# Optimization experiments

Hardware: AMD Instinct MI355X
Metric: run time of the kernel (lower is better)

The kernel has to match this reference:

```python
import jax, jax.numpy as jnp
import numpy as np

HEADS = 8
MEM_LEN = 32


def _mha(q, k, v, Wq, bq, Wk, bk, Wv, bv, Wo, bo):
    # torch nn.MultiheadAttention, batch_first=False. q: [Lq,B,E], k/v: [Lk,B,E]
    Lq, B, E = q.shape
    d = E // HEADS

    def proj(t, W, b):
        p = t @ W.T + b
        return p.reshape(t.shape[0], B, HEADS, d).transpose(1, 2, 0, 3)  # [B,h,L,d]

    qh, kh, vh = proj(q, Wq, bq), proj(k, Wk, bk), proj(v, Wv, bv)
    scale = 1.0 / jnp.sqrt(jnp.asarray(d, q.dtype))
    att = jax.nn.softmax(jnp.einsum('bhqd,bhkd->bhqk', qh * scale, kh), axis=-1)
    out = jnp.einsum('bhqk,bhkd->bhqd', att, vh)          # [B,h,Lq,d]
    out = out.transpose(2, 0, 1, 3).reshape(Lq, B, E)
    return out @ Wo.T + bo


def _forward(x, h, c, memK, memV, externalK, externalV,
             W_ih, W_hh, b_ih, b_hh,
             sWq, sbq, sWk, sbk, sWv, sbv, sWo, sbo,
             cWq, cbq, cWk, cbk, cWv, cbv, cWo, cbo,
             Wres, bres, Wrout, brout, Wcomp, bcomp, Wexp, bexp, Wgate, bgate):
    H = h.shape[1]
    # LSTMCell (torch gate order i, f, g, o)
    gates = x @ W_ih.T + b_ih + h @ W_hh.T + b_hh
    i, f, g, o = jnp.split(gates, 4, axis=1)
    c_next = jax.nn.sigmoid(f) * c + jax.nn.sigmoid(i) * jnp.tanh(g)
    h_lstm = jax.nn.sigmoid(o) * jnp.tanh(c_next)
    # append detached h_lstm to short memory, keep last MEM_LEN entries
    cur = jax.lax.stop_gradient(h_lstm)[None]                      # [1,B,H]
    memK_new = jnp.concatenate([memK, cur], axis=0)[-MEM_LEN:]     # [ML,B,H]
    memV_new = jnp.concatenate([memV, cur], axis=0)[-MEM_LEN:]
    qSelf = h_lstm[None]                                           # [1,B,H]
    self_out = _mha(qSelf, memK_new, memV_new, sWq, sbq, sWk, sbk, sWv, sbv, sWo, sbo)[0]
    ext_out = _mha(qSelf, externalK, externalV, cWq, cbq, cWk, cbk, cWv, cbv, cWo, cbo)[0]
    rw = jax.nn.softmax(h_lstm @ Wrout.T + brout, axis=1)          # [B,2] router
    routed_attn = rw[:, :1] * self_out + rw[:, 1:2] * ext_out
    routed = h_lstm + routed_attn + routed_attn @ Wres.T + bres
    temporal_summary = memK_new.mean(axis=0)                       # [B,H]
    compressed = temporal_summary @ Wcomp.T + bcomp                # [B,H//4]
    expanded = compressed @ Wexp.T + bexp                          # [B,H]
    reps = -(-H // compressed.shape[1])
    compressed_expanded = jnp.tile(compressed, (1, reps))[:, :H]
    gate = jax.nn.sigmoid(jnp.concatenate([x, routed], axis=1) @ Wgate.T + bgate)
    hCT = compressed_expanded + gate * (expanded - compressed_expanded)  # torch.lerp
    hFinal = (h_lstm + routed + hCT) / 3.0                         # dropout = identity (eval)
    return hFinal, h_lstm, c_next


def setup_inputs() -> dict:
    key = jax.random.key(0)
    ks = jax.random.split(key, 34)
    B, I, H, ML, EL = 2048, 1024, 1024, 32, 32
    BN = H // 4
    rn = lambda k, s, sc=1.0: jax.random.normal(k, s, dtype=jnp.float32) * sc
    return {
        'x': rn(ks[0], (B, I)), 'h': rn(ks[1], (B, H)), 'c': rn(ks[2], (B, H)),
        'memK': rn(ks[3], (ML, B, H)), 'memV': rn(ks[4], (ML, B, H)),
        'externalK': rn(ks[5], (EL, B, H)), 'externalV': rn(ks[6], (EL, B, H)),
        'W_ih': rn(ks[7], (4 * H, I), 0.02), 'W_hh': rn(ks[8], (4 * H, H), 0.02),
        'b_ih': jnp.zeros((4 * H,), jnp.float32), 'b_hh': jnp.zeros((4 * H,), jnp.float32),
        'sWq': rn(ks[9], (H, H), 0.02), 'sbq': rn(ks[10], (H,), 0.02),
        'sWk': rn(ks[11], (H, H), 0.02), 'sbk': rn(ks[12], (H,), 0.02),
        'sWv': rn(ks[13], (H, H), 0.02), 'sbv': rn(ks[14], (H,), 0.02),
        'sWo': rn(ks[15], (H, H), 0.02), 'sbo': rn(ks[16], (H,), 0.02),
        'cWq': rn(ks[17], (H, H), 0.02), 'cbq': rn(ks[18], (H,), 0.02),
        'cWk': rn(ks[19], (H, H), 0.02), 'cbk': rn(ks[20], (H,), 0.02),
        'cWv': rn(ks[21], (H, H), 0.02), 'cbv': rn(ks[22], (H,), 0.02),
        'cWo': rn(ks[23], (H, H), 0.02), 'cbo': rn(ks[24], (H,), 0.02),
        'Wres': rn(ks[25], (H, H), 0.02), 'bres': rn(ks[26], (H,), 0.02),
        'Wrout': rn(ks[27], (2, H), 0.02), 'brout': rn(ks[28], (2,), 0.02),
        'Wcomp': rn(ks[29], (BN, H), 0.02), 'bcomp': rn(ks[30], (BN,), 0.02),
        'Wexp': rn(ks[31], (H, BN), 0.02), 'bexp': rn(ks[32], (H,), 0.02),
        'Wgate': rn(ks[33], (H, I + H), 0.02), 'bgate': jnp.zeros((H,), jnp.float32),
    }


def reference(x, h, c, memK, memV, externalK, externalV,
              W_ih, W_hh, b_ih, b_hh,
              sWq, sbq, sWk, sbk, sWv, sbv, sWo, sbo,
              cWq, cbq, cWk, cbk, cWv, cbv, cWo, cbo,
              Wres, bres, Wrout, brout, Wcomp, bcomp, Wexp, bexp, Wgate, bgate):
    return _forward(x, h, c, memK, memV, externalK, externalV,
                    W_ih, W_hh, b_ih, b_hh,
                    sWq, sbq, sWk, sbk, sWv, sbv, sWo, sbo,
                    cWq, cbq, cWk, cbk, cWv, cbv, cWo, cbo,
                    Wres, bres, Wrout, brout, Wcomp, bcomp, Wexp, bexp, Wgate, bgate)
```

## Files before the change

kernel.cpp:

```cpp
#include <hip/hip_runtime.h>
#include <math.h>

typedef __attribute__((ext_vector_type(4))) float f32x4;
typedef __attribute__((ext_vector_type(8))) short bf16x8;
typedef __attribute__((ext_vector_type(4))) unsigned short u16x4;

__device__ __forceinline__ unsigned short f2bf(float f) {
  unsigned u = __builtin_bit_cast(unsigned, f);
  u += 0x7fffu + ((u >> 16) & 1u);
  return (unsigned short)(u >> 16);
}
__device__ __forceinline__ float bf2f(unsigned short s) {
  return __builtin_bit_cast(float, (unsigned)s << 16);
}
__device__ __forceinline__ float sigmoidf_(float x) { return 1.f / (1.f + __expf(-x)); }

template <int TN, int ACAT, int BCAT, int EPI, int ABF16, int OBF16>
__global__ __launch_bounds__(256) void gemm_k(
    const void* __restrict__ A1, const void* __restrict__ A1b, int lda1, long aZ,
    const void* __restrict__ A2, int lda2, int Ksplit,
    const float* __restrict__ B1, const float* __restrict__ B1b, int ldb1, long bZ,
    const float* __restrict__ B2, int ldb2,
    const float* __restrict__ bias1, const float* __restrict__ bias1b, long biasZ,
    const float* __restrict__ bias2,
    void* __restrict__ C, void* __restrict__ Cb, int ldc, long cZ,
    int K, int zs, float scale,
    const float* __restrict__ P0, const float* __restrict__ P1,
    const float* __restrict__ P2, const float* __restrict__ P3) {
  constexpr int NBI = TN / 32;
  __shared__ unsigned short As[2][128][32];
  __shared__ unsigned short Bs[2][TN][32];
  const int t = threadIdx.x;
  const int lane = t & 63;
  const int wave = t >> 6;
  const int wr = wave >> 1, wc = wave & 1;

  const unsigned gx = gridDim.x, gy = gridDim.y;
  unsigned L = blockIdx.x + gx * (blockIdx.y + gy * blockIdx.z);
  const unsigned nwg = gx * gy * gridDim.z;
  L = (L & 7u) * (nwg >> 3) + (L >> 3);
  const int bn = L % gx;
  const unsigned r1 = L / gx;
  const int bm = r1 % gy;
  const int z = r1 / gy;

  const bool hi = z >= zs;
  const int zz = hi ? z - zs : z;
  const char* Abase = (const char*)(hi ? A1b : A1) + (long)zz * aZ * (ABF16 ? 2 : 4);
  const float* Bbase = (hi ? B1b : B1) + (long)zz * bZ;
  const float* biasp = hi ? bias1b : bias1;
  char* Czc = (char*)(hi ? Cb : C) + (long)zz * cZ * (OBF16 ? 2 : 4);

  const int ar = t >> 3;
  const int bc = (t & 7) * 4;

  const int kIters = K >> 5;
  u16x4 Ra[4], Rb[NBI];

  auto loadT = [&](int kt) {
    const int k0 = kt << 5;
    const char* Ap; int ldA, kA;
    if (ACAT == 1 && k0 >= Ksplit) { Ap = (const char*)A2; ldA = lda2; kA = k0 - Ksplit; }
    else { Ap = Abase; ldA = lda1; kA = k0; }
    const float* Bp; int ldB, kB;
    if (BCAT == 1 && k0 >= Ksplit) { Bp = B2; ldB = ldb2; kB = k0 - Ksplit; }
    else { Bp = Bbase; ldB = ldb1; kB = k0; }
#pragma unroll
    for (int i = 0; i < 4; ++i) {
      const long aoff = ((long)bm * 128 + ar + 32 * i) * ldA + kA + bc;
      if (ABF16) {
        Ra[i] = *(const u16x4*)((const unsigned short*)Ap + aoff);
      } else {
        f32x4 v = *(const f32x4*)((const float*)Ap + aoff);
        u16x4 pk;
        pk[0] = f2bf(v[0]); pk[1] = f2bf(v[1]); pk[2] = f2bf(v[2]); pk[3] = f2bf(v[3]);
        Ra[i] = pk;
      }
    }
#pragma unroll
    for (int i = 0; i < NBI; ++i) {
      f32x4 bv = *(const f32x4*)(Bp + ((long)bn * TN + ar + 32 * i) * ldB + kB + bc);
      u16x4 bp;
      bp[0] = f2bf(bv[0]); bp[1] = f2bf(bv[1]); bp[2] = f2bf(bv[2]); bp[3] = f2bf(bv[3]);
      Rb[i] = bp;
    }
  };

  loadT(0);

  f32x4 acc[4][NBI] = {};
  int p = 0;
  for (int kt = 0; kt < kIters; ++kt) {
    __syncthreads();
#pragma unroll
    for (int i = 0; i < 4; ++i) *(u16x4*)&As[p][ar + 32 * i][bc] = Ra[i];
#pragma unroll
    for (int i = 0; i < NBI; ++i) *(u16x4*)&Bs[p][ar + 32 * i][bc] = Rb[i];
    if (kt + 1 < kIters) loadT(kt + 1);
    __syncthreads();

    bf16x8 af[4], bfr[NBI];
#pragma unroll
    for (int mi = 0; mi < 4; ++mi)
      af[mi] = *(const bf16x8*)&As[p][wr * 64 + mi * 16 + (lane & 15)][(lane >> 4) * 8];
#pragma unroll
    for (int ni = 0; ni < NBI; ++ni)
      bfr[ni] = *(const bf16x8*)&Bs[p][wc * (TN / 2) + ni * 16 + (lane & 15)][(lane >> 4) * 8];
#pragma unroll
    for (int mi = 0; mi < 4; ++mi)
#pragma unroll
      for (int ni = 0; ni < NBI; ++ni)
        acc[mi][ni] = __builtin_amdgcn_mfma_f32_16x16x32_bf16(af[mi], bfr[ni], acc[mi][ni], 0, 0, 0);
    p ^= 1;
  }

  const int colb = bn * TN + wc * (TN / 2);
  const int rowb = bm * 128 + wr * 64;
#pragma unroll
  for (int mi = 0; mi < 4; ++mi) {
#pragma unroll
    for (int ni = 0; ni < NBI; ++ni) {
      f32x4 v = acc[mi][ni];
      const int col = colb + ni * 16 + (lane & 15);
      const int row0 = rowb + mi * 16 + ((lane >> 4) << 2);
      float bsum = 0.f;
      if (biasp) bsum += biasp[zz * biasZ + col];
      if (bias2) bsum += bias2[col];
#pragma unroll
      for (int q = 0; q < 4; ++q) {
        const long row = row0 + q;
        const long off = row * ldc + col;
        const float val = v[q] + bsum;
        if (EPI == 0) {
          if (OBF16) ((unsigned short*)Czc)[off] = f2bf(val * scale);
          else       ((float*)Czc)[off] = val * scale;
        } else if (EPI == 1) {
          ((float*)Czc)[off] = val + P0[off] + P1[off];
        } else if (EPI == 2) {
          const float g = sigmoidf_(val);
          const float ce = P0[row * 256 + (col & 255)];
          const float ex = P1[off];
          ((float*)Czc)[off] = (P2[off] + P3[off] + ce + g * (ex - ce)) * (1.f / 3.f);
        } else if (EPI == 3) {
          ((unsigned short*)Czc)[off] = f2bf(val * P0[2 * row + (hi ? 1 : 0)]);
        } else {
          ((float*)Czc)[off] = val + P2[2 * row] * P0[col] + P2[2 * row + 1] * P1[col];
        }
      }
    }
  }
}

__global__ __launch_bounds__(256) void transpose_k(const float* __restrict__ in0,
                                                   float* __restrict__ out0,
                                                   const float* __restrict__ in1,
                                                   float* __restrict__ out1, int n) {
  __shared__ float tile[64][65];
  const float* in = blockIdx.z ? in1 : in0;
  float* out = blockIdx.z ? out1 : out0;
  const int tr = blockIdx.y, tc = blockIdx.x, t = threadIdx.x;
#pragma unroll
  for (int it = 0; it < 16; ++it) {
    int idx = t + 256 * it;
    int r = idx >> 6, c = idx & 63;
    tile[r][c] = in[(long)(tr * 64 + r) * n + tc * 64 + c];
  }
  __syncthreads();
#pragma unroll
  for (int it = 0; it < 16; ++it) {
    int idx = t + 256 * it;
    int rr = idx >> 6, cc = idx & 63;
    out[(long)(tc * 64 + rr) * n + tr * 64 + cc] = tile[cc][rr];
  }
}

__global__ __launch_bounds__(256) void lstm_k(const float* __restrict__ gates,
                                              const float* __restrict__ c_in,
                                              const float* __restrict__ Wr,
                                              const float* __restrict__ br,
                                              float* __restrict__ c_out,
                                              float* __restrict__ h_ws,
                                              float* __restrict__ h_out,
                                              float* __restrict__ rw) {
  const int b = blockIdx.x, t = threadIdx.x;
  const long base = (long)b * 1024 + t * 4;
  const float* gb = gates + (long)b * 4096 + t * 4;
  f32x4 gi = *(const f32x4*)(gb);
  f32x4 gf = *(const f32x4*)(gb + 1024);
  f32x4 gg = *(const f32x4*)(gb + 2048);
  f32x4 go = *(const f32x4*)(gb + 3072);
  f32x4 cv = *(const f32x4*)(c_in + base);
  f32x4 cn, hv;
#pragma unroll
  for (int q = 0; q < 4; ++q) {
    float cc = sigmoidf_(gf[q]) * cv[q] + sigmoidf_(gi[q]) * tanhf(gg[q]);
    cn[q] = cc;
    hv[q] = sigmoidf_(go[q]) * tanhf(cc);
  }
  *(f32x4*)(c_out + base) = cn;
  *(f32x4*)(h_ws + base) = hv;
  *(f32x4*)(h_out + base) = hv;
  f32x4 w0 = *(const f32x4*)(Wr + t * 4);
  f32x4 w1 = *(const f32x4*)(Wr + 1024 + t * 4);
  float a0 = hv[0] * w0[0] + hv[1] * w0[1] + hv[2] * w0[2] + hv[3] * w0[3];
  float a1 = hv[0] * w1[0] + hv[1] * w1[1] + hv[2] * w1[2] + hv[3] * w1[3];
#pragma unroll
  for (int m = 32; m >= 1; m >>= 1) {
    a0 += __shfl_xor(a0, m);
    a1 += __shfl_xor(a1, m);
  }
  __shared__ float red[8];
  if ((t & 63) == 0) { red[t >> 6] = a0; red[4 + (t >> 6)] = a1; }
  __syncthreads();
  if (t == 0) {
    float z0 = red[0] + red[1] + red[2] + red[3] + br[0];
    float z1 = red[4] + red[5] + red[6] + red[7] + br[1];
    float mx = fmaxf(z0, z1);
    float e0 = __expf(z0 - mx), e1 = __expf(z1 - mx);
    float s = e0 + e1;
    rw[2 * b] = e0 / s;
    rw[2 * b + 1] = e1 / s;
  }
}

__global__ __launch_bounds__(256) void attn4_k(
    const float* __restrict__ memK, const float* __restrict__ memV,
    const float* __restrict__ extK, const float* __restrict__ extV,
    const float* __restrict__ hl,
    const unsigned short* __restrict__ qtS, const unsigned short* __restrict__ qtE,
    unsigned short* __restrict__ mixS, unsigned short* __restrict__ mixE,
    float* __restrict__ ts) {
  const int NB = 2048, H = 1024;
  __shared__ __align__(16) unsigned short LDSU[38912];
  __shared__ __align__(16) unsigned short P_lds[16 * 36];
  const int b = blockIdx.x;
  const bool self = blockIdx.y == 0;
  const int t = threadIdx.x, lane = t & 63, w = t >> 6;

  auto krow = [&](int r) -> const float* {
    return self ? ((r < 31) ? memK + ((long)(r + 1) * NB + b) * H : hl + (long)b * H)
                : extK + ((long)r * NB + b) * H;
  };
  auto vrow = [&](int r) -> const float* {
    return self ? ((r < 31) ? memV + ((long)(r + 1) * NB + b) * H : hl + (long)b * H)
                : extV + ((long)r * NB + b) * H;
  };

  const int chS = t >> 5, c4S = t & 31;
  const unsigned kbase = (unsigned)(chS * 4 + (c4S >> 3)) * 1168 + (unsigned)(c4S & 7) * 4;
#pragma unroll
  for (int g = 0; g < 4; ++g) {
    f32x4 R[8];
#pragma unroll
    for (int u = 0; u < 8; ++u) R[u] = *(const f32x4*)(krow(g * 8 + u) + t * 4);
#pragma unroll
    for (int u = 0; u < 8; ++u) {
      const int r = g * 8 + u;
      u16x4 pk;
      pk[0] = f2bf(R[u][0]); pk[1] = f2bf(R[u][1]); pk[2] = f2bf(R[u][2]); pk[3] = f2bf(R[u][3]);
      *(u16x4*)&LDSU[kbase + (unsigned)r * 36] = pk;
    }
  }
  __syncthreads();

  if (self) {
#pragma unroll
    for (int ci = 0; ci < 4; ++ci) {
      const int g = t + 256 * ci;
      const int q = g & 127;
      const unsigned short* base = &LDSU[(unsigned)((g >> 7) * 4 + (q >> 5)) * 1168 + (q & 31)];
      float s = 0.f;
#pragma unroll
      for (int r = 0; r < 32; ++r) s += bf2f(base[r * 36]);
      ts[(long)b * H + g] = s * (1.f / 32.f);
    }
  }

  const unsigned short* qtb =
      (self ? qtS : qtE) + (long)b * 8192 + (long)(lane & 7) * 1024 + (lane >> 4) * 8;
  f32x4 accS[2] = {};
  for (int jj = 0; jj < 32; ++jj) {
    bf16x8 bq = *(const bf16x8*)(qtb + jj * 32);
#pragma unroll
    for (int mi = 0; mi < 2; ++mi) {
      const unsigned short* ap =
          &LDSU[(unsigned)jj * 1168 + (unsigned)(mi * 16 + (lane & 15)) * 36 + (lane >> 4) * 8];
      union { unsigned long long q[2]; bf16x8 v; } ua;
      ua.q[0] = *(const unsigned long long*)ap;
      ua.q[1] = *(const unsigned long long*)(ap + 4);
      accS[mi] = __builtin_amdgcn_mfma_f32_16x16x32_bf16(ua.v, bq, accS[mi], 0, 0, 0);
    }
  }

  {
    float mx = -3.4e38f;
#pragma unroll
    for (int mi = 0; mi < 2; ++mi)
#pragma unroll
      for (int q = 0; q < 4; ++q) mx = fmaxf(mx, accS[mi][q]);
    mx = fmaxf(mx, __shfl_xor(mx, 16));
    mx = fmaxf(mx, __shfl_xor(mx, 32));
    float sum = 0.f;
    float pv[2][4];
#pragma unroll
    for (int mi = 0; mi < 2; ++mi)
#pragma unroll
      for (int q = 0; q < 4; ++q) { pv[mi][q] = __expf(accS[mi][q] - mx); sum += pv[mi][q]; }
    sum += __shfl_xor(sum, 16);
    sum += __shfl_xor(sum, 32);
    const float rinv = 1.f / sum;
    const bool valid = (lane & 15) < 8;
#pragma unroll
    for (int mi = 0; mi < 2; ++mi) {
      u16x4 pk;
#pragma unroll
      for (int q = 0; q < 4; ++q) pk[q] = valid ? f2bf(pv[mi][q] * rinv) : (unsigned short)0;
      *(u16x4*)&P_lds[(unsigned)(lane & 15) * 36 + mi * 16 + (lane >> 4) * 4] = pk;
    }
  }
  __syncthreads();

#pragma unroll
  for (int g = 0; g < 4; ++g) {
    f32x4 RA[4], RB[4];
#pragma unroll
    for (int u = 0; u < 4; ++u) {
      const int pr = g * 4 + u;
      RA[u] = *(const f32x4*)(vrow(2 * pr) + t * 4);
      RB[u] = *(const f32x4*)(vrow(2 * pr + 1) + t * 4);
    }
#pragma unroll
    for (int u = 0; u < 4; ++u) {
      const int pr = g * 4 + u;
#pragma unroll
      for (int e = 0; e < 4; ++e) {
        const unsigned dw = (unsigned)f2bf(RA[u][e]) | ((unsigned)f2bf(RB[u][e]) << 16);
        *(unsigned*)&LDSU[(unsigned)(t * 4 + e) * 38 + 2 * pr] = dw;
      }
    }
  }
  __syncthreads();

  bf16x8 pa = *(const bf16x8*)&P_lds[(unsigned)(lane & 15) * 36 + (lane >> 4) * 8];
  unsigned short* mixp = (self ? mixS : mixE) + (long)b * 8192;
#pragma unroll
  for (int ch = 0; ch < 8; ++ch) {
#pragma unroll
    for (int i = 0; i < 2; ++i) {
      const int dbase = ch * 128 + w * 32 + i * 16;
      const unsigned* vb =
          (const unsigned*)&LDSU[(unsigned)(dbase + (lane & 15)) * 38 + (lane >> 4) * 8];
      union { unsigned u[4]; bf16x8 v; } uu;
      uu.u[0] = vb[0]; uu.u[1] = vb[1]; uu.u[2] = vb[2]; uu.u[3] = vb[3];
      f32x4 o = __builtin_amdgcn_mfma_f32_16x16x32_bf16(pa, uu.v, (f32x4){0.f, 0.f, 0.f, 0.f},
                                                        0, 0, 0);
      if (lane < 32) {
        const int d = dbase + (lane & 15);
        const int h0 = (lane >> 4) * 4;
#pragma unroll
        for (int q = 0; q < 4; ++q) mixp[(long)(h0 + q) * 1024 + d] = f2bf(o[q]);
      }
    }
  }
}

extern "C" void kernel_launch(void* const* d_in, const int* in_sizes, int n_in,
                              void* d_out, int out_size, void* d_ws, size_t ws_size,
                              hipStream_t stream) {
  const float* x    = (const float*)d_in[0];
  const float* h    = (const float*)d_in[1];
  const float* c    = (const float*)d_in[2];
  const float* memK = (const float*)d_in[3];
  const float* memV = (const float*)d_in[4];
  const float* extK = (const float*)d_in[5];
  const float* extV = (const float*)d_in[6];
  const float* W_ih = (const float*)d_in[7];
  const float* W_hh = (const float*)d_in[8];
  const float* b_ih = (const float*)d_in[9];
  const float* b_hh = (const float*)d_in[10];
  const float* sWq = (const float*)d_in[11];
  const float* sbq = (const float*)d_in[12];
  const float* sWk = (const float*)d_in[13];
  const float* sWv = (const float*)d_in[15];
  const float* sbv = (const float*)d_in[16];
  const float* sWo = (const float*)d_in[17];
  const float* sbo = (const float*)d_in[18];
  const float* cWq = (const float*)d_in[19];
  const float* cbq = (const float*)d_in[20];
  const float* cWk = (const float*)d_in[21];
  const float* cWv = (const float*)d_in[23];
  const float* cbv = (const float*)d_in[24];
  const float* cWo = (const float*)d_in[25];
  const float* cbo = (const float*)d_in[26];
  const float* Wres = (const float*)d_in[27];
  const float* bres = (const float*)d_in[28];
  const float* Wrout = (const float*)d_in[29];
  const float* brout = (const float*)d_in[30];
  const float* Wcomp = (const float*)d_in[31];
  const float* bcomp = (const float*)d_in[32];
  const float* Wexp = (const float*)d_in[33];
  const float* bexp = (const float*)d_in[34];
  const float* Wgate = (const float*)d_in[35];
  const float* bgate = (const float*)d_in[36];
  (void)in_sizes; (void)n_in; (void)out_size; (void)ws_size;

  float* out = (float*)d_out;
  float* w = (float*)d_ws;
  const long M1 = 1024 * 1024;
  float* gates   = w;
  float* hl      = w + 8 * M1;
  unsigned short* qsS = (unsigned short*)(w + 10 * M1);
  unsigned short* qsE = (unsigned short*)(w + 12 * M1);
  float* wkTs    = w + 14 * M1;
  float* wkTc    = w + 15 * M1;
  unsigned short* qtS = (unsigned short*)(w + 16 * M1);
  unsigned short* qtE = (unsigned short*)(w + 32 * M1);
  unsigned short* mixS = (unsigned short*)(w + 48 * M1);
  unsigned short* mixE = (unsigned short*)(w + 64 * M1);
  float* ts      = w + 80 * M1;
  unsigned short* attnS = (unsigned short*)(w + 82 * M1);
  unsigned short* attnE = (unsigned short*)(w + 84 * M1);
  float* rw      = w + 90 * M1;
  float* rattn   = w + 91 * M1;
  float* routed  = w + 93 * M1;
  float* comp    = w + 95 * M1;
  float* expd    = w + 96 * M1;

  float* hFinal_out = out;
  float* hl_out     = out + 2 * M1;
  float* cn_out     = out + 4 * M1;

  const float scaleq = 0.08838834764831845f;
  const int ZBIG = 1 << 30;
  dim3 blk(256);
  const float* nf = nullptr;

  gemm_k<128, 1, 1, 0, 0, 0><<<dim3(32, 16, 1), blk, 0, stream>>>(
      x, nullptr, 1024, 0, h, 1024, 1024,
      W_ih, nf, 1024, 0, W_hh, 1024,
      b_ih, nf, 0, b_hh,
      gates, nullptr, 4096, 0,
      2048, ZBIG, 1.f, nf, nf, nf, nf);

  transpose_k<<<dim3(16, 16, 2), blk, 0, stream>>>(sWk, wkTs, cWk, wkTc, 1024);

  lstm_k<<<2048, blk, 0, stream>>>(gates, c, Wrout, brout, cn_out, hl, hl_out, rw);

  gemm_k<128, 0, 0, 0, 0, 1><<<dim3(8, 16, 2), blk, 0, stream>>>(
      hl, hl, 1024, 0, nullptr, 0, 0,
      sWq, cWq, 1024, 0, nf, 0,
      sbq, cbq, 0, nf,
      qsS, qsE, 1024, 0,
      1024, 1, scaleq, nf, nf, nf, nf);

  gemm_k<128, 0, 0, 0, 1, 1><<<dim3(8, 16, 16), blk, 0, stream>>>(
      qsS, qsE, 1024, 128, nullptr, 0, 0,
      wkTs, wkTc, 1024, 128, nf, 0,
      nf, nf, 0, nf,
      qtS, qtE, 8192, 1024,
      128, 8, 1.f, nf, nf, nf, nf);

  attn4_k<<<dim3(2048, 2), blk, 0, stream>>>(memK, memV, extK, extV, hl,
                                             qtS, qtE, mixS, mixE, ts);

  gemm_k<64, 0, 0, 3, 1, 1><<<dim3(2, 16, 16), blk, 0, stream>>>(
      mixS, mixE, 8192, 1024, nullptr, 0, 0,
      sWv, cWv, 1024, 131072, nf, 0,
      sbv, cbv, 128, nf,
      attnS, attnE, 1024, 128,
      1024, 8, 1.f, rw, nf, nf, nf);

  gemm_k<64, 1, 1, 4, 1, 0><<<dim3(16, 16, 1), blk, 0, stream>>>(
      attnS, nullptr, 1024, 0, attnE, 1024, 1024,
      sWo, nf, 1024, 0, cWo, 1024,
      nf, nf, 0, nf,
      rattn, nullptr, 1024, 0,
      2048, ZBIG, 1.f, sbo, cbo, rw, nf);

  gemm_k<64, 0, 0, 1, 0, 0><<<dim3(16, 16, 1), blk, 0, stream>>>(
      rattn, nullptr, 1024, 0, nullptr, 0, 0,
      Wres, nf, 1024, 0, nf, 0,
      bres, nf, 0, nf,
      routed, nullptr, 1024, 0,
      1024, ZBIG, 1.f, hl, rattn, nf, nf);

  gemm_k<64, 0, 0, 0, 0, 0><<<dim3(4, 16, 1), blk, 0, stream>>>(
      ts, nullptr, 1024, 0, nullptr, 0, 0,
      Wcomp, nf, 1024, 0, nf, 0,
      bcomp, nf, 0, nf,
      comp, nullptr, 256, 0,
      1024, ZBIG, 1.f, nf, nf, nf, nf);
  gemm_k<64, 0, 0, 0, 0, 0><<<dim3(16, 16, 1), blk, 0, stream>>>(
      comp, nullptr, 256, 0, nullptr, 0, 0,
      Wexp, nf, 256, 0, nf, 0,
      bexp, nf, 0, nf,
      expd, nullptr, 1024, 0,
      256, ZBIG, 1.f, nf, nf, nf, nf);

  gemm_k<64, 1, 0, 2, 0, 0><<<dim3(16, 16, 1), blk, 0, stream>>>(
      x, nullptr, 1024, 0, routed, 1024, 1024,
      Wgate, nf, 2048, 0, nf, 0,
      bgate, nf, 0, nf,
      hFinal_out, nullptr, 1024, 0,
      2048, ZBIG, 1.f, comp, expd, hl, routed);
}
```

Baseline: 792.5 us.

## Replace MFMA attention kernel with fp32 FMA attention reading K/V directly

The per-batch attention kernel no longer stages K and V into LDS as bf16 for MFMA. The query is expanded to fp32 in LDS, scores are computed by threads that each own a K row with shuffle reductions, and P·V is accumulated in fp32 registers straight from global V, with coalesced bf16 stores. This drops the LDS transpose and bf16 conversion work and the padded MFMA tiles, at the cost of more VALU FMAs and an extra pass over K for the temporal mean. Precision also rises to fp32 for scores and the weighted sum.

```diff
diff --git a/kernel.cpp b/kernel.cpp
--- a/kernel.cpp
+++ b/kernel.cpp
@@ -4,6 +4,7 @@
 typedef __attribute__((ext_vector_type(4))) float f32x4;
 typedef __attribute__((ext_vector_type(8))) short bf16x8;
 typedef __attribute__((ext_vector_type(4))) unsigned short u16x4;
+typedef __attribute__((ext_vector_type(8))) unsigned short u16x8;
 
 __device__ __forceinline__ unsigned short f2bf(float f) {
   unsigned u = __builtin_bit_cast(unsigned, f);
@@ -223,7 +224,7 @@
   }
 }
 
-__global__ __launch_bounds__(256) void attn4_k(
+__global__ __launch_bounds__(256) void attn5_k(
     const float* __restrict__ memK, const float* __restrict__ memV,
     const float* __restrict__ extK, const float* __restrict__ extV,
     const float* __restrict__ hl,
@@ -231,136 +232,116 @@
     unsigned short* __restrict__ mixS, unsigned short* __restrict__ mixE,
     float* __restrict__ ts) {
   const int NB = 2048, H = 1024;
-  __shared__ __align__(16) unsigned short LDSU[38912];
-  __shared__ __align__(16) unsigned short P_lds[16 * 36];
+  __shared__ float qtf[8][1028];
+  __shared__ float S_lds[32][8];
+  __shared__ float P_lds[32][8];
   const int b = blockIdx.x;
   const bool self = blockIdx.y == 0;
-  const int t = threadIdx.x, lane = t & 63, w = t >> 6;
-
-  auto krow = [&](int r) -> const float* {
-    return self ? ((r < 31) ? memK + ((long)(r + 1) * NB + b) * H : hl + (long)b * H)
-                : extK + ((long)r * NB + b) * H;
+  const int t = threadIdx.x;
+
+  auto krow = [&](int r_) -> const float* {
+    return self ? ((r_ < 31) ? memK + ((long)(r_ + 1) * NB + b) * H : hl + (long)b * H)
+                : extK + ((long)r_ * NB + b) * H;
   };
-  auto vrow = [&](int r) -> const float* {
-    return self ? ((r < 31) ? memV + ((long)(r + 1) * NB + b) * H : hl + (long)b * H)
-                : extV + ((long)r * NB + b) * H;
+  auto vrow = [&](int r_) -> const float* {
+    return self ? ((r_ < 31) ? memV + ((long)(r_ + 1) * NB + b) * H : hl + (long)b * H)
+                : extV + ((long)r_ * NB + b) * H;
   };
 
-  const int chS = t >> 5, c4S = t & 31;
-  const unsigned kbase = (unsigned)(chS * 4 + (c4S >> 3)) * 1168 + (unsigned)(c4S & 7) * 4;
-#pragma unroll
-  for (int g = 0; g < 4; ++g) {
-    f32x4 R[8];
-#pragma unroll
-    for (int u = 0; u < 8; ++u) R[u] = *(const f32x4*)(krow(g * 8 + u) + t * 4);
-#pragma unroll
-    for (int u = 0; u < 8; ++u) {
-      const int r = g * 8 + u;
-      u16x4 pk;
-      pk[0] = f2bf(R[u][0]); pk[1] = f2bf(R[u][1]); pk[2] = f2bf(R[u][2]); pk[3] = f2bf(R[u][3]);
-      *(u16x4*)&LDSU[kbase + (unsigned)r * 36] = pk;
+  {
+    const unsigned short* qtb = (self ? qtS : qtE) + (long)b * 8192;
+#pragma unroll
+    for (int i = 0; i < 4; ++i) {
+      const int idx = t + 256 * i;
+      u16x8 qv = *(const u16x8*)(qtb + idx * 8);
+      const int hh = idx >> 7, pos = (idx & 127) * 8;
+      f32x4 lo, hi2;
+      lo[0] = bf2f(qv[0]); lo[1] = bf2f(qv[1]); lo[2] = bf2f(qv[2]); lo[3] = bf2f(qv[3]);
+      hi2[0] = bf2f(qv[4]); hi2[1] = bf2f(qv[5]); hi2[2] = bf2f(qv[6]); hi2[3] = bf2f(qv[7]);
+      *(f32x4*)&qtf[hh][pos] = lo;
+      *(f32x4*)&qtf[hh][pos + 4] = hi2;
     }
   }
   __syncthreads();
 
+  const int r = t >> 3, sub = t & 7;
+  const float* Kr = krow(r) + sub * 4;
+  float s[8] = {};
+#pragma unroll
+  for (int j = 0; j < 32; j += 4) {
+    f32x4 kc[4];
+#pragma unroll
+    for (int u = 0; u < 4; ++u) kc[u] = *(const f32x4*)(Kr + (j + u) * 32);
+#pragma unroll
+    for (int u = 0; u < 4; ++u) {
+      const int kk = ((j + u) * 8 + sub) * 4;
+#pragma unroll
+      for (int hh = 0; hh < 8; ++hh) {
+        f32x4 q = *(const f32x4*)&qtf[hh][kk];
+        s[hh] += kc[u][0] * q[0] + kc[u][1] * q[1] + kc[u][2] * q[2] + kc[u][3] * q[3];
+      }
+    }
+  }
+#pragma unroll
+  for (int hh = 0; hh < 8; ++hh) {
+    s[hh] += __shfl_xor(s[hh], 1);
+    s[hh] += __shfl_xor(s[hh], 2);
+    s[hh] += __shfl_xor(s[hh], 4);
+  }
+  if (sub == 0) {
+#pragma unroll
+    for (int hh = 0; hh < 8; ++hh) S_lds[r][hh] = s[hh];
+  }
+  __syncthreads();
+
+  {
+    const int rr = t & 31, hh = t >> 5;
+    float Sv = S_lds[rr][hh];
+    float mx = Sv;
+#pragma unroll
+    for (int m = 16; m >= 1; m >>= 1) mx = fmaxf(mx, __shfl_xor(mx, m, 32));
+    float pr = __expf(Sv - mx);
+    float su = pr;
+#pragma unroll
+    for (int m = 16; m >= 1; m >>= 1) su += __shfl_xor(su, m, 32);
+    P_lds[rr][hh] = pr / su;
+  }
+  __syncthreads();
+
   if (self) {
-#pragma unroll
-    for (int ci = 0; ci < 4; ++ci) {
-      const int g = t + 256 * ci;
-      const int q = g & 127;
-      const unsigned short* base = &LDSU[(unsigned)((g >> 7) * 4 + (q >> 5)) * 1168 + (q & 31)];
-      float s = 0.f;
-#pragma unroll
-      for (int r = 0; r < 32; ++r) s += bf2f(base[r * 36]);
-      ts[(long)b * H + g] = s * (1.f / 32.f);
-    }
-  }
-
-  const unsigned short* qtb =
-      (self ? qtS : qtE) + (long)b * 8192 + (long)(lane & 7) * 1024 + (lane >> 4) * 8;
-  f32x4 accS[2] = {};
-  for (int jj = 0; jj < 32; ++jj) {
-    bf16x8 bq = *(const bf16x8*)(qtb + jj * 32);
-#pragma unroll
-    for (int mi = 0; mi < 2; ++mi) {
-      const unsigned short* ap =
-          &LDSU[(unsigned)jj * 1168 + (unsigned)(mi * 16 + (lane & 15)) * 36 + (lane >> 4) * 8];
-      union { unsigned long long q[2]; bf16x8 v; } ua;
-      ua.q[0] = *(const unsigned long long*)ap;
-      ua.q[1] = *(const unsigned long long*)(ap + 4);
-      accS[mi] = __builtin_amdgcn_mfma_f32_16x16x32_bf16(ua.v, bq, accS[mi], 0, 0, 0);
-    }
-  }
-
-  {
-    float mx = -3.4e38f;
-#pragma unroll
-    for (int mi = 0; mi < 2; ++mi)
-#pragma unroll
-      for (int q = 0; q < 4; ++q) mx = fmaxf(mx, accS[mi][q]);
-    mx = fmaxf(mx, __shfl_xor(mx, 16));
-    mx = fmaxf(mx, __shfl_xor(mx, 32));
-    float sum = 0.f;
-    float pv[2][4];
-#pragma unroll
-    for (int mi = 0; mi < 2; ++mi)
-#pragma unroll
-      for (int q = 0; q < 4; ++q) { pv[mi][q] = __expf(accS[mi][q] - mx); sum += pv[mi][q]; }
-    sum += __shfl_xor(sum, 16);
-    sum += __shfl_xor(sum, 32);
-    const float rinv = 1.f / sum;
-    const bool valid = (lane & 15) < 8;
-#pragma unroll
-    for (int mi = 0; mi < 2; ++mi) {
-      u16x4 pk;
-#pragma unroll
-      for (int q = 0; q < 4; ++q) pk[q] = valid ? f2bf(pv[mi][q] * rinv) : (unsigned short)0;
-      *(u16x4*)&P_lds[(unsigned)(lane & 15) * 36 + mi * 16 + (lane >> 4) * 4] = pk;
-    }
-  }
-  __syncthreads();
-
-#pragma unroll
-  for (int g = 0; g < 4; ++g) {
-    f32x4 RA[4], RB[4];
+    f32x4 a = {};
+#pragma unroll
+    for (int l = 0; l < 32; ++l) {
+      f32x4 kv = *(const f32x4*)(krow(l) + 4 * t);
+      a += kv;
+    }
+    *(f32x4*)(ts + (long)b * H + 4 * t) = a * (1.f / 32.f);
+  }
+
+  f32x4 acc[8] = {};
+#pragma unroll
+  for (int l = 0; l < 32; l += 4) {
+    f32x4 vv[4];
+#pragma unroll
+    for (int u = 0; u < 4; ++u) vv[u] = *(const f32x4*)(vrow(l + u) + 4 * t);
 #pragma unroll
     for (int u = 0; u < 4; ++u) {
-      const int pr = g * 4 + u;
-      RA[u] = *(const f32x4*)(vrow(2 * pr) + t * 4);
-      RB[u] = *(const f32x4*)(vrow(2 * pr + 1) + t * 4);
-    }
-#pragma unroll
-    for (int u = 0; u < 4; ++u) {
-      const int pr = g * 4 + u;
-#pragma unroll
-      for (int e = 0; e < 4; ++e) {
-        const unsigned dw = (unsigned)f2bf(RA[u][e]) | ((unsigned)f2bf(RB[u][e]) << 16);
-        *(unsigned*)&LDSU[(unsigned)(t * 4 + e) * 38 + 2 * pr] = dw;
+      f32x4 pa = *(const f32x4*)&P_lds[l + u][0];
+      f32x4 pb = *(const f32x4*)&P_lds[l + u][4];
+#pragma unroll
+      for (int hh = 0; hh < 4; ++hh) {
+        acc[hh] += pa[hh] * vv[u];
+        acc[4 + hh] += pb[hh] * vv[u];
       }
     }
   }
-  __syncthreads();
-
-  bf16x8 pa = *(const bf16x8*)&P_lds[(unsigned)(lane & 15) * 36 + (lane >> 4) * 8];
   unsigned short* mixp = (self ? mixS : mixE) + (long)b * 8192;
 #pragma unroll
-  for (int ch = 0; ch < 8; ++ch) {
-#pragma unroll
-    for (int i = 0; i < 2; ++i) {
-      const int dbase = ch * 128 + w * 32 + i * 16;
-      const unsigned* vb =
-          (const unsigned*)&LDSU[(unsigned)(dbase + (lane & 15)) * 38 + (lane >> 4) * 8];
-      union { unsigned u[4]; bf16x8 v; } uu;
-      uu.u[0] = vb[0]; uu.u[1] = vb[1]; uu.u[2] = vb[2]; uu.u[3] = vb[3];
-      f32x4 o = __builtin_amdgcn_mfma_f32_16x16x32_bf16(pa, uu.v, (f32x4){0.f, 0.f, 0.f, 0.f},
-                                                        0, 0, 0);
-      if (lane < 32) {
-        const int d = dbase + (lane & 15);
-        const int h0 = (lane >> 4) * 4;
-#pragma unroll
-        for (int q = 0; q < 4; ++q) mixp[(long)(h0 + q) * 1024 + d] = f2bf(o[q]);
-      }
-    }
+  for (int hh = 0; hh < 8; ++hh) {
+    u16x4 pk;
+    pk[0] = f2bf(acc[hh][0]); pk[1] = f2bf(acc[hh][1]);
+    pk[2] = f2bf(acc[hh][2]); pk[3] = f2bf(acc[hh][3]);
+    *(u16x4*)(mixp + hh * 1024 + 4 * t) = pk;
   }
 }
 
@@ -460,7 +441,7 @@
       qtS, qtE, 8192, 1024,
       128, 8, 1.f, nf, nf, nf, nf);
 
-  attn4_k<<<dim3(2048, 2), blk, 0, stream>>>(memK, memV, extK, extV, hl,
+  attn5_k<<<dim3(2048, 2), blk, 0, stream>>>(memK, memV, extK, extV, hl,
                                              qtS, qtE, mixS, mixE, ts);
 
   gemm_k<64, 0, 0, 3, 1, 1><<<dim3(2, 16, 16), blk, 0, stream>>>(
```

Result: no change. 807.4 us (+1.9%).
